# Kernel optimization log

Hardware: AMD Instinct MI355X
Metric: run time of the kernel (lower is better)

Reference implementation:

```python
import jax, jax.numpy as jnp
import numpy as np

T, OBS, MLP, H, ACT = 2048, 512, 1024, 1024, 16
SIG0 = 0.5  # config['noise_std'] -> NoisyLinear init_std


def mish(x):
    return x * jnp.tanh(jax.nn.softplus(x))


def noisy_linear(x, wm, ws, bm, bs, kw, kb):
    # NoisyLinear: perturbed weights/bias sampled per forward call from the key.
    # In the original, the same key is tiled across the vmapped time axis, so a
    # single noise sample is shared by all timesteps -> one sample here.
    w = wm + ws * jax.random.normal(kw, wm.shape, wm.dtype)
    b = bm + bs * jax.random.normal(kb, bm.shape, bm.dtype)
    return x @ w.T + b


def setup_inputs() -> dict:
    key = jax.random.key(0)
    ks = jax.random.split(key, 8)

    def lin(k, o, i):
        lim = 1.0 / np.sqrt(i)
        return jax.random.uniform(k, (o, i), jnp.float32, -lim, lim)

    return {
        "x": jax.random.normal(ks[0], (T, OBS), jnp.float32),
        "state": jnp.zeros((H,), jnp.float32),
        "start": jax.random.randint(ks[1], (T,), 0, 2, dtype=jnp.int32),
        "done": jnp.zeros((T,), jnp.int32),
        "pre_wm": lin(ks[2], MLP, OBS),
        "pre_ws": jnp.full((MLP, OBS), SIG0, jnp.float32),
        "pre_bm": jnp.zeros((MLP,), jnp.float32),
        "pre_bs": jnp.full((MLP,), SIG0, jnp.float32),
        "gru_wih": lin(ks[3], 3 * H, MLP),
        "gru_whh": lin(ks[4], 3 * H, H),
        "gru_b": jnp.zeros((3 * H,), jnp.float32),
        "gru_bn": jnp.zeros((H,), jnp.float32),
        "p1_wm": lin(ks[5], MLP, H),
        "p1_ws": jnp.full((MLP, H), SIG0, jnp.float32),
        "p1_bm": jnp.zeros((MLP,), jnp.float32),
        "p1_bs": jnp.full((MLP,), SIG0, jnp.float32),
        "p2_wm": lin(ks[6], MLP, MLP),
        "p2_ws": jnp.full((MLP, MLP), SIG0, jnp.float32),
        "p2_bm": jnp.zeros((MLP,), jnp.float32),
        "p2_bs": jnp.full((MLP,), SIG0, jnp.float32),
        "p3_wm": lin(ks[7], ACT, MLP) * 0.01,  # final_layer_init: small last layer
        "p3_ws": jnp.full((ACT, MLP), SIG0, jnp.float32),
        "p3_bm": jnp.zeros((ACT,), jnp.float32),
        "p3_bs": jnp.full((ACT,), SIG0, jnp.float32),
    }


def _forward(x, state, start, pre_wm, pre_ws, pre_bm, pre_bs, gru_wih, gru_whh,
             gru_b, gru_bn, p1_wm, p1_ws, p1_bm, p1_bs, p2_wm, p2_ws, p2_bm,
             p2_bs, p3_wm, p3_ws, p3_bm, p3_bs):
    nk = jax.random.split(jax.random.key(7), 8)
    # pre MLP: NoisyLinear + mish, vectorized over time
    z = mish(noisy_linear(x, pre_wm, pre_ws, pre_bm, pre_bs, nk[0], nk[1]))  # [T, MLP]
    # input-side GRU gates precomputed as one big GEMM (equinox GRUCell math)
    igates = z @ gru_wih.T + gru_b  # [T, 3H]
    keep = (1 - start).astype(z.dtype)  # [T]; 0 where an episode starts -> reset h

    def step(h, inp):
        ig, k = inp
        h_in = h * k  # state * logical_not(start)
        hg = h_in @ gru_whh.T  # [3H]
        ir, iz, in_ = jnp.split(ig, 3)
        hr, hz, hn = jnp.split(hg, 3)
        r = jax.nn.sigmoid(ir + hr)
        u = jax.nn.sigmoid(iz + hz)
        n = jnp.tanh(in_ + r * (hn + gru_bn))
        h_new = n + u * (h_in - n)  # == (1-u)*n + u*h_in
        return h_new, h_new

    final_state, states = jax.lax.scan(step, state, (igates, keep))  # states: [T, H]
    # post MLP: NoisyLinear+mish, NoisyLinear+mish, NoisyLinear (final)
    y = mish(noisy_linear(states, p1_wm, p1_ws, p1_bm, p1_bs, nk[2], nk[3]))
    y = mish(noisy_linear(y, p2_wm, p2_ws, p2_bm, p2_bs, nk[4], nk[5]))
    y = noisy_linear(y, p3_wm, p3_ws, p3_bm, p3_bs, nk[6], nk[7])  # [T, ACT]
    return y, final_state


def reference(x, state, start, done, pre_wm, pre_ws, pre_bm, pre_bs, gru_wih,
              gru_whh, gru_b, gru_bn, p1_wm, p1_ws, p1_bm, p1_bs, p2_wm, p2_ws,
              p2_bm, p2_bs, p3_wm, p3_ws, p3_bm, p3_bs):
    del done  # threaded through the scan in the original but never used
    return _forward(x, state, start, pre_wm, pre_ws, pre_bm, pre_bs, gru_wih,
                    gru_whh, gru_b, gru_bn, p1_wm, p1_ws, p1_bm, p1_bs, p2_wm,
                    p2_ws, p2_bm, p2_bs, p3_wm, p3_ws, p3_bm, p3_bs)
```

## Files before the change

### kernel.cpp

```cpp
#include <hip/hip_runtime.h>
#include <hip/hip_cooperative_groups.h>
#include <cstdint>
#include <cstddef>

namespace cg = cooperative_groups;

#define T_ 2048
#define OBS_ 512
#define MLP_ 1024
#define H_ 1024
#define ACT_ 16
#define H3_ 3072

typedef short bf16x8 __attribute__((ext_vector_type(8)));
typedef float f32x4 __attribute__((ext_vector_type(4)));

__host__ __device__ __forceinline__ uint32_t rotl32(uint32_t v, int d) {
  return (v << d) | (v >> (32 - d));
}
__host__ __device__ __forceinline__ void tf2x32(uint32_t k0, uint32_t k1,
                                                uint32_t x0, uint32_t x1,
                                                uint32_t& o0, uint32_t& o1) {
  uint32_t ks2 = k0 ^ k1 ^ 0x1BD11BDAu;
  x0 += k0; x1 += k1;
  x0 += x1; x1 = rotl32(x1, 13); x1 ^= x0;
  x0 += x1; x1 = rotl32(x1, 15); x1 ^= x0;
  x0 += x1; x1 = rotl32(x1, 26); x1 ^= x0;
  x0 += x1; x1 = rotl32(x1, 6);  x1 ^= x0;
  x0 += k1; x1 += ks2 + 1u;
  x0 += x1; x1 = rotl32(x1, 17); x1 ^= x0;
  x0 += x1; x1 = rotl32(x1, 29); x1 ^= x0;
  x0 += x1; x1 = rotl32(x1, 16); x1 ^= x0;
  x0 += x1; x1 = rotl32(x1, 24); x1 ^= x0;
  x0 += ks2; x1 += k0 + 2u;
  x0 += x1; x1 = rotl32(x1, 13); x1 ^= x0;
  x0 += x1; x1 = rotl32(x1, 15); x1 ^= x0;
  x0 += x1; x1 = rotl32(x1, 26); x1 ^= x0;
  x0 += x1; x1 = rotl32(x1, 6);  x1 ^= x0;
  x0 += k0; x1 += k1 + 3u;
  x0 += x1; x1 = rotl32(x1, 17); x1 ^= x0;
  x0 += x1; x1 = rotl32(x1, 29); x1 ^= x0;
  x0 += x1; x1 = rotl32(x1, 16); x1 ^= x0;
  x0 += x1; x1 = rotl32(x1, 24); x1 ^= x0;
  x0 += k1; x1 += ks2 + 4u;
  x0 += x1; x1 = rotl32(x1, 13); x1 ^= x0;
  x0 += x1; x1 = rotl32(x1, 15); x1 ^= x0;
  x0 += x1; x1 = rotl32(x1, 26); x1 ^= x0;
  x0 += x1; x1 = rotl32(x1, 6);  x1 ^= x0;
  x0 += ks2; x1 += k0 + 5u;
  o0 = x0; o1 = x1;
}

__device__ __forceinline__ float erfinv_f32(float x) {
  float w = -log1pf(-x * x);
  float p;
  if (w < 5.0f) {
    w = w - 2.5f;
    p = 2.81022636e-08f;
    p = fmaf(p, w, 3.43273939e-07f);
    p = fmaf(p, w, -3.5233877e-06f);
    p = fmaf(p, w, -4.39150654e-06f);
    p = fmaf(p, w, 0.00021858087f);
    p = fmaf(p, w, -0.00125372503f);
    p = fmaf(p, w, -0.00417768164f);
    p = fmaf(p, w, 0.246640727f);
    p = fmaf(p, w, 1.50140941f);
  } else {
    w = sqrtf(w) - 3.0f;
    p = -0.000200214257f;
    p = fmaf(p, w, 0.000100950558f);
    p = fmaf(p, w, 0.00134934322f);
    p = fmaf(p, w, -0.00367342844f);
    p = fmaf(p, w, 0.00573950773f);
    p = fmaf(p, w, -0.0076224613f);
    p = fmaf(p, w, 0.00943887047f);
    p = fmaf(p, w, 1.00167406f);
    p = fmaf(p, w, 2.83297682f);
  }
  return p * x;
}

__device__ __forceinline__ float bits_to_normal(uint32_t bits) {
  const float lo = -0.99999994f;
  float f = __uint_as_float((bits >> 9) | 0x3f800000u) - 1.0f;
  float u = fmaf(f, 2.0f, lo);
  u = fmaxf(lo, u);
  return 1.41421356237f * erfinv_f32(u);
}

__device__ __forceinline__ float sigmoidf_(float x) {
  return 1.0f / (1.0f + expf(-x));
}
__device__ __forceinline__ float mishf_(float x) {
  float sp = fmaxf(x, 0.0f) + log1pf(expf(-fabsf(x)));
  return x * tanhf(sp);
}

__device__ __forceinline__ ushort f2bf(float v) {
  uint32_t u = __float_as_uint(v);
  uint32_t r = (u + 0x7FFFu + ((u >> 16) & 1u)) >> 16;
  return (ushort)r;
}
__device__ __forceinline__ float bf2f(ushort b) {
  return __uint_as_float(((uint32_t)b) << 16);
}

struct NoiseDesc {
  const float* wm; const float* ws;
  ushort* dh; ushort* dl; float* df;
  uint32_t k0, k1, base, mode;
};
struct NoiseArgs { NoiseDesc d[8]; uint32_t total; int* meta_zero; };

__global__ __launch_bounds__(256) void k_gen_noise(NoiseArgs a) {
  if (blockIdx.x < 16) a.meta_zero[blockIdx.x * 256 + threadIdx.x] = 0;
  uint32_t idx = blockIdx.x * 256u + threadIdx.x;
  for (; idx < a.total; idx += gridDim.x * 256u) {
    int ti = 0;
#pragma unroll
    for (int i = 1; i < 8; ++i) if (idx >= a.d[i].base) ti = i;
    NoiseDesc dd = a.d[ti];
    uint32_t j = idx - dd.base;
    uint32_t b1, b2;
    tf2x32(dd.k0, dd.k1, 0u, j, b1, b2);
    float v = fmaf(dd.ws[j], bits_to_normal(b1 ^ b2), dd.wm[j]);
    if (dd.mode) {
      ushort hb = f2bf(v);
      dd.dh[j] = hb;
      dd.dl[j] = f2bf(v - bf2f(hb));
    } else {
      dd.df[j] = v;
    }
  }
}

__global__ __launch_bounds__(256) void k_split(const float* __restrict__ in,
                                               ushort* __restrict__ h,
                                               ushort* __restrict__ l, int n4) {
  int i = blockIdx.x * 256 + threadIdx.x;
  if (i >= n4) return;
  float4 v = ((const float4*)in)[i];
  ushort4 hb, lb;
  hb.x = f2bf(v.x); lb.x = f2bf(v.x - bf2f(hb.x));
  hb.y = f2bf(v.y); lb.y = f2bf(v.y - bf2f(hb.y));
  hb.z = f2bf(v.z); lb.z = f2bf(v.z - bf2f(hb.z));
  hb.w = f2bf(v.w); lb.w = f2bf(v.w - bf2f(hb.w));
  ((ushort4*)h)[i] = hb;
  ((ushort4*)l)[i] = lb;
}

template <int ACTF, int OUTM>
__global__ __launch_bounds__(256, 2) void k_mgemm(
    const ushort* __restrict__ Ah, const ushort* __restrict__ Al,
    const ushort* __restrict__ Wh, const ushort* __restrict__ Wl,
    const float* __restrict__ bias,
    float* __restrict__ Cf, ushort* __restrict__ Ch, ushort* __restrict__ Cl,
    int K, int Nreal, int ldc) {
  __shared__ ushort sA[2][128 * 32];
  __shared__ ushort sW[2][128 * 32];
  const int tid = threadIdx.x;
  const int m0 = blockIdx.y * 128, n0 = blockIdx.x * 128;
  const int wid = tid >> 6, lane = tid & 63;
  const int wm = (wid >> 1) * 64, wn = (wid & 1) * 64;
  const int lr = lane & 15, lk = lane >> 4;
  const int r0 = tid >> 2;
  const int c0 = (tid & 3) * 8;
  f32x4 acc[4][4] = {};
  for (int k0 = 0; k0 < K; k0 += 32) {
    const size_t aoff0 = (size_t)(m0 + r0) * K + k0 + c0;
    const size_t aoff1 = (size_t)(m0 + r0 + 64) * K + k0 + c0;
    const size_t woff0 = (size_t)(n0 + r0) * K + k0 + c0;
    const size_t woff1 = (size_t)(n0 + r0 + 64) * K + k0 + c0;
    int4 ah0 = *(const int4*)(Ah + aoff0);
    int4 ah1 = *(const int4*)(Ah + aoff1);
    int4 al0 = *(const int4*)(Al + aoff0);
    int4 al1 = *(const int4*)(Al + aoff1);
    int4 wh0 = *(const int4*)(Wh + woff0);
    int4 wh1 = *(const int4*)(Wh + woff1);
    int4 wl0 = *(const int4*)(Wl + woff0);
    int4 wl1 = *(const int4*)(Wl + woff1);
    __syncthreads();
    *(int4*)(&sA[0][r0 * 32 + c0]) = ah0;
    *(int4*)(&sA[0][(r0 + 64) * 32 + c0]) = ah1;
    *(int4*)(&sA[1][r0 * 32 + c0]) = al0;
    *(int4*)(&sA[1][(r0 + 64) * 32 + c0]) = al1;
    *(int4*)(&sW[0][r0 * 32 + c0]) = wh0;
    *(int4*)(&sW[0][(r0 + 64) * 32 + c0]) = wh1;
    *(int4*)(&sW[1][r0 * 32 + c0]) = wl0;
    *(int4*)(&sW[1][(r0 + 64) * 32 + c0]) = wl1;
    __syncthreads();
    bf16x8 fah[4], fal[4], fwh[4], fwl[4];
#pragma unroll
    for (int f = 0; f < 4; ++f) {
      int ar = (wm + f * 16 + lr) * 32 + lk * 8;
      fah[f] = *(const bf16x8*)(&sA[0][ar]);
      fal[f] = *(const bf16x8*)(&sA[1][ar]);
      int wr = (wn + f * 16 + lr) * 32 + lk * 8;
      fwh[f] = *(const bf16x8*)(&sW[0][wr]);
      fwl[f] = *(const bf16x8*)(&sW[1][wr]);
    }
#pragma unroll
    for (int mf = 0; mf < 4; ++mf)
#pragma unroll
      for (int nf = 0; nf < 4; ++nf) {
        acc[mf][nf] = __builtin_amdgcn_mfma_f32_16x16x32_bf16(fah[mf], fwh[nf], acc[mf][nf], 0, 0, 0);
        acc[mf][nf] = __builtin_amdgcn_mfma_f32_16x16x32_bf16(fah[mf], fwl[nf], acc[mf][nf], 0, 0, 0);
        acc[mf][nf] = __builtin_amdgcn_mfma_f32_16x16x32_bf16(fal[mf], fwh[nf], acc[mf][nf], 0, 0, 0);
      }
  }
#pragma unroll
  for (int mf = 0; mf < 4; ++mf)
#pragma unroll
    for (int nf = 0; nf < 4; ++nf) {
      int col = n0 + wn + nf * 16 + lr;
      if (col >= Nreal) continue;
      float bv = bias[col];
#pragma unroll
      for (int r = 0; r < 4; ++r) {
        int row = m0 + wm + mf * 16 + lk * 4 + r;
        float v = acc[mf][nf][r] + bv;
        if (ACTF) v = mishf_(v);
        if (OUTM == 0) {
          Cf[(size_t)row * ldc + col] = v;
        } else {
          ushort hb = f2bf(v);
          Ch[(size_t)row * ldc + col] = hb;
          Cl[(size_t)row * ldc + col] = f2bf(v - bf2f(hb));
        }
      }
    }
}

struct SMemScan {
  union {
    struct {
      ushort Hs[2][64][40];
      ushort Bs[2][96][40];
    } mm;
    int scan[2][2048];
  } u;
  int tl[64];
};

__global__ __launch_bounds__(256) void k_scan(
    const float* __restrict__ ig, const float* __restrict__ whh,
    const float* __restrict__ gbn, const float* __restrict__ state0,
    const int* __restrict__ start, int* __restrict__ counts,
    int* __restrict__ cursors, int* __restrict__ li_,
    int* __restrict__ offsets, int* __restrict__ list,
    ushort* __restrict__ st_h, ushort* __restrict__ st_l,
    float* __restrict__ hg0) {
  cg::grid_group grid = cg::this_grid();
  __shared__ SMemScan sm;
  const int tid = threadIdx.x, bid = blockIdx.x, nb = gridDim.x;
  const float keep0 = 1.0f - (float)start[0];

  if (bid < 8) {
    int t = bid * 256 + tid;
    int l = 0, tt = t;
    while (tt > 0 && start[tt] == 0) { tt--; l++; }
    li_[t] = l;
    if (t > 0) atomicAdd(&counts[l], 1);
  }
  grid.sync();

  if (bid == 0) {
    for (int i = tid; i < 2048; i += 256) sm.u.scan[0][i] = counts[i];
    __syncthreads();
    int cur = 0;
    for (int d = 1; d < 2048; d <<= 1) {
      int nx = cur ^ 1;
      for (int i = tid; i < 2048; i += 256)
        sm.u.scan[nx][i] = sm.u.scan[cur][i] + (i >= d ? sm.u.scan[cur][i - d] : 0);
      __syncthreads();
      cur = nx;
    }
    for (int i = tid; i < 2048; i += 256)
      offsets[i] = (i == 0) ? 0 : sm.u.scan[cur][i - 1];
  }
  grid.sync();

  if (bid < 8) {
    int t = bid * 256 + tid;
    if (t > 0) {
      int l = li_[t];
      int pos = atomicAdd(&cursors[l], 1);
      list[offsets[l] + pos] = t;
    }
  }
  {
    int gw = bid * 4 + (tid >> 6);
    int lane = tid & 63;
    for (int r = gw * 3; r < gw * 3 + 3 && r < H3_; ++r) {
      const float* wr = whh + (size_t)r * H_;
      float s = 0.f;
      for (int c = lane; c < H_; c += 64) s = fmaf(wr[c], state0[c] * keep0, s);
      for (int o = 32; o; o >>= 1) s += __shfl_down(s, o, 64);
      if (lane == 0) hg0[r] = s;
    }
  }
  grid.sync();

  {
    int cnt0 = counts[0];
    int off0 = offsets[0];
    int total = (cnt0 + 1) * H_;
    for (int e = bid * 256 + tid; e < total; e += nb * 256) {
      int s = e >> 10, i = e & (H_ - 1);
      int t; float hin, hr, hz, hn;
      if (s == 0) {
        t = 0; hin = state0[i] * keep0;
        hr = hg0[i]; hz = hg0[H_ + i]; hn = hg0[2 * H_ + i];
      } else {
        t = list[off0 + s - 1]; hin = 0.f; hr = 0.f; hz = 0.f; hn = 0.f;
      }
      float ir = ig[(size_t)t * H3_ + i];
      float iz = ig[(size_t)t * H3_ + H_ + i];
      float in_ = ig[(size_t)t * H3_ + 2 * H_ + i];
      float r = sigmoidf_(ir + hr), u = sigmoidf_(iz + hz);
      float n = tanhf(in_ + r * (hn + gbn[i]));
      float v = n + u * (hin - n);
      ushort hb = f2bf(v);
      st_h[(size_t)t * H_ + i] = hb;
      st_l[(size_t)t * H_ + i] = f2bf(v - bf2f(hb));
    }
  }
  grid.sync();

  const int wid = tid >> 6, lane = tid & 63;
  const int lr = lane & 15, lk = lane >> 4;
  const int wm = (wid >> 1) * 32;
  const int wi = wid & 1;

  for (int k = 1; k < 2048; ++k) {
    int cnt = counts[k];
    if (cnt == 0) break;
    int off = offsets[k];
    int mtiles = (cnt + 63) >> 6;
    int tiles = mtiles << 5;
    for (int tile = bid; tile < tiles; tile += nb) {
      int mt = tile >> 5;
      int i0 = (tile & 31) << 5;
      __syncthreads();
      if (tid < 64) {
        int s = mt * 64 + tid;
        sm.tl[tid] = (s < cnt) ? list[off + s] : 0;
      }
      __syncthreads();

      f32x4 acc[2][3] = {};
      int4 pa[2]; float4 pb[3];
      const int a_koct = tid & 3, a_row = (tid >> 2) & 63;
      const int b_kq0 = tid & 7, b_row0 = tid >> 3;
      const int b_kq1 = (tid + 256) & 7, b_row1 = (tid + 256) >> 3;
      const int b_kq2 = (tid + 512) & 7, b_row2 = (tid + 512) >> 3;
      const size_t brow_off0 = (size_t)(((b_row0 >> 5) * H_) + i0 + (b_row0 & 31)) * H_;
      const size_t brow_off1 = (size_t)(((b_row1 >> 5) * H_) + i0 + (b_row1 & 31)) * H_;
      const size_t brow_off2 = (size_t)(((b_row2 >> 5) * H_) + i0 + (b_row2 & 31)) * H_;

#define LOADA(K0, DST)                                                        \
      {                                                                       \
        int t0_ = sm.tl[a_row];                                               \
        DST[0] = make_int4(0, 0, 0, 0); DST[1] = make_int4(0, 0, 0, 0);       \
        if (t0_ > 0) {                                                        \
          size_t base_ = (size_t)(t0_ - 1) * H_ + (K0) + a_koct * 8;          \
          DST[0] = *(const int4*)(st_h + base_);                              \
          DST[1] = *(const int4*)(st_l + base_);                              \
        }                                                                     \
      }
#define LOADB(K0, DST)                                                        \
      {                                                                       \
        DST[0] = *(const float4*)(whh + brow_off0 + (K0) + b_kq0 * 4);        \
        DST[1] = *(const float4*)(whh + brow_off1 + (K0) + b_kq1 * 4);        \
        DST[2] = *(const float4*)(whh + brow_off2 + (K0) + b_kq2 * 4);        \
      }

      LOADA(0, pa); LOADB(0, pb);
      for (int k0 = 0; k0 < H_; k0 += 32) {
        __syncthreads();
        *(int4*)(&sm.u.mm.Hs[0][a_row][a_koct * 8]) = pa[0];
        *(int4*)(&sm.u.mm.Hs[1][a_row][a_koct * 8]) = pa[1];
        {
          ushort4 hb, lb;
          float4 w = pb[0];
          hb.x = f2bf(w.x); lb.x = f2bf(w.x - bf2f(hb.x));
          hb.y = f2bf(w.y); lb.y = f2bf(w.y - bf2f(hb.y));
          hb.z = f2bf(w.z); lb.z = f2bf(w.z - bf2f(hb.z));
          hb.w = f2bf(w.w); lb.w = f2bf(w.w - bf2f(hb.w));
          *(ushort4*)(&sm.u.mm.Bs[0][b_row0][b_kq0 * 4]) = hb;
          *(ushort4*)(&sm.u.mm.Bs[1][b_row0][b_kq0 * 4]) = lb;
          w = pb[1];
          hb.x = f2bf(w.x); lb.x = f2bf(w.x - bf2f(hb.x));
          hb.y = f2bf(w.y); lb.y = f2bf(w.y - bf2f(hb.y));
          hb.z = f2bf(w.z); lb.z = f2bf(w.z - bf2f(hb.z));
          hb.w = f2bf(w.w); lb.w = f2bf(w.w - bf2f(hb.w));
          *(ushort4*)(&sm.u.mm.Bs[0][b_row1][b_kq1 * 4]) = hb;
          *(ushort4*)(&sm.u.mm.Bs[1][b_row1][b_kq1 * 4]) = lb;
          w = pb[2];
          hb.x = f2bf(w.x); lb.x = f2bf(w.x - bf2f(hb.x));
          hb.y = f2bf(w.y); lb.y = f2bf(w.y - bf2f(hb.y));
          hb.z = f2bf(w.z); lb.z = f2bf(w.z - bf2f(hb.z));
          hb.w = f2bf(w.w); lb.w = f2bf(w.w - bf2f(hb.w));
          *(ushort4*)(&sm.u.mm.Bs[0][b_row2][b_kq2 * 4]) = hb;
          *(ushort4*)(&sm.u.mm.Bs[1][b_row2][b_kq2 * 4]) = lb;
        }
        int4 na[2] = {pa[0], pa[1]};
        float4 nb[3] = {pb[0], pb[1], pb[2]};
        if (k0 + 32 < H_) { LOADA(k0 + 32, na); LOADB(k0 + 32, nb); }
        __syncthreads();
        bf16x8 ah[2], al[2], bh[3], bl[3];
#pragma unroll
        for (int mf = 0; mf < 2; ++mf) {
          int row = wm + mf * 16 + lr;
          ah[mf] = *(const bf16x8*)(&sm.u.mm.Hs[0][row][lk * 8]);
          al[mf] = *(const bf16x8*)(&sm.u.mm.Hs[1][row][lk * 8]);
        }
#pragma unroll
        for (int g = 0; g < 3; ++g) {
          int row = g * 32 + wi * 16 + lr;
          bh[g] = *(const bf16x8*)(&sm.u.mm.Bs[0][row][lk * 8]);
          bl[g] = *(const bf16x8*)(&sm.u.mm.Bs[1][row][lk * 8]);
        }
#pragma unroll
        for (int mf = 0; mf < 2; ++mf)
#pragma unroll
          for (int g = 0; g < 3; ++g) {
            acc[mf][g] = __builtin_amdgcn_mfma_f32_16x16x32_bf16(ah[mf], bh[g], acc[mf][g], 0, 0, 0);
            acc[mf][g] = __builtin_amdgcn_mfma_f32_16x16x32_bf16(ah[mf], bl[g], acc[mf][g], 0, 0, 0);
            acc[mf][g] = __builtin_amdgcn_mfma_f32_16x16x32_bf16(al[mf], bh[g], acc[mf][g], 0, 0, 0);
          }
        pa[0] = na[0]; pa[1] = na[1];
        pb[0] = nb[0]; pb[1] = nb[1]; pb[2] = nb[2];
      }
#undef LOADA
#undef LOADB
      int i = i0 + wi * 16 + lr;
#pragma unroll
      for (int mf = 0; mf < 2; ++mf)
#pragma unroll
        for (int r = 0; r < 4; ++r) {
          int slot = wm + mf * 16 + lk * 4 + r;
          int t = sm.tl[slot];
          if (t <= 0) continue;
          size_t pidx = (size_t)(t - 1) * H_ + i;
          float hin = bf2f(st_h[pidx]) + bf2f(st_l[pidx]);
          float ir = ig[(size_t)t * H3_ + i];
          float iz = ig[(size_t)t * H3_ + H_ + i];
          float in_ = ig[(size_t)t * H3_ + 2 * H_ + i];
          float rr = sigmoidf_(ir + acc[mf][0][r]);
          float uu = sigmoidf_(iz + acc[mf][1][r]);
          float nn = tanhf(in_ + rr * (acc[mf][2][r] + gbn[i]));
          float v = nn + uu * (hin - nn);
          ushort hb = f2bf(v);
          st_h[(size_t)t * H_ + i] = hb;
          st_l[(size_t)t * H_ + i] = f2bf(v - bf2f(hb));
        }
    }
    grid.sync();
  }
}

__global__ void k_final(const ushort* __restrict__ st_h,
                        const ushort* __restrict__ st_l,
                        float* __restrict__ out) {
  int i = blockIdx.x * 256 + threadIdx.x;
  if (i < H_)
    out[T_ * ACT_ + i] = bf2f(st_h[(size_t)(T_ - 1) * H_ + i]) +
                         bf2f(st_l[(size_t)(T_ - 1) * H_ + i]);
}

extern "C" void kernel_launch(void* const* d_in, const int* in_sizes, int n_in,
                              void* d_out, int out_size, void* d_ws, size_t ws_size,
                              hipStream_t stream) {
  const float* x      = (const float*)d_in[0];
  const float* state0 = (const float*)d_in[1];
  const int*   start  = (const int*)d_in[2];
  const float* pre_wm = (const float*)d_in[4];
  const float* pre_ws = (const float*)d_in[5];
  const float* pre_bm = (const float*)d_in[6];
  const float* pre_bs = (const float*)d_in[7];
  const float* gru_wih = (const float*)d_in[8];
  const float* gru_whh = (const float*)d_in[9];
  const float* gru_b  = (const float*)d_in[10];
  const float* gru_bn = (const float*)d_in[11];
  const float* p1_wm = (const float*)d_in[12];
  const float* p1_ws = (const float*)d_in[13];
  const float* p1_bm = (const float*)d_in[14];
  const float* p1_bs = (const float*)d_in[15];
  const float* p2_wm = (const float*)d_in[16];
  const float* p2_ws = (const float*)d_in[17];
  const float* p2_bm = (const float*)d_in[18];
  const float* p2_bs = (const float*)d_in[19];
  const float* p3_wm = (const float*)d_in[20];
  const float* p3_ws = (const float*)d_in[21];
  const float* p3_bm = (const float*)d_in[22];
  const float* p3_bs = (const float*)d_in[23];

  char* p = (char*)d_ws;
  auto nxt = [&](size_t bytes) { char* r = p; p += (bytes + 255) & ~255ul; return r; };
  ushort* wihh = (ushort*)nxt((size_t)H3_ * MLP_ * 2);
  ushort* wihl = (ushort*)nxt((size_t)H3_ * MLP_ * 2);
  ushort* preWh = (ushort*)nxt((size_t)MLP_ * OBS_ * 2);
  ushort* preWl = (ushort*)nxt((size_t)MLP_ * OBS_ * 2);
  ushort* p1Wh = (ushort*)nxt((size_t)MLP_ * H_ * 2);
  ushort* p1Wl = (ushort*)nxt((size_t)MLP_ * H_ * 2);
  ushort* p2Wh = (ushort*)nxt((size_t)MLP_ * MLP_ * 2);
  ushort* p2Wl = (ushort*)nxt((size_t)MLP_ * MLP_ * 2);
  ushort* p3Wh = (ushort*)nxt((size_t)128 * MLP_ * 2);
  ushort* p3Wl = (ushort*)nxt((size_t)128 * MLP_ * 2);
  float* preB = (float*)nxt(MLP_ * 4);
  float* p1B  = (float*)nxt(MLP_ * 4);
  float* p2B  = (float*)nxt(MLP_ * 4);
  float* p3B  = (float*)nxt(ACT_ * 4);
  ushort* B1h = (ushort*)nxt((size_t)T_ * MLP_ * 2);
  ushort* B1l = (ushort*)nxt((size_t)T_ * MLP_ * 2);
  ushort* B2h = (ushort*)nxt((size_t)T_ * MLP_ * 2);
  ushort* B2l = (ushort*)nxt((size_t)T_ * MLP_ * 2);
  float* igb = (float*)nxt((size_t)T_ * H3_ * 4);
  float* hg0 = (float*)nxt(H3_ * 4);
  int* counts  = (int*)nxt(2048 * 4);
  int* cursors = (int*)nxt(2048 * 4);
  int* li      = (int*)nxt(2048 * 4);
  int* offsets = (int*)nxt(2048 * 4);
  int* list    = (int*)nxt(2048 * 4);

  uint32_t nk0[8], nk1[8];
  for (int i = 0; i < 8; ++i) {
    uint32_t b1, b2;
    tf2x32(0u, 7u, 0u, (uint32_t)i, b1, b2);
    nk0[i] = b1; nk1[i] = b2;
  }

  NoiseArgs na;
  const float* wms[8] = {pre_wm, pre_bm, p1_wm, p1_bm, p2_wm, p2_bm, p3_wm, p3_bm};
  const float* wss[8] = {pre_ws, pre_bs, p1_ws, p1_bs, p2_ws, p2_bs, p3_ws, p3_bs};
  ushort* dhs[8] = {preWh, nullptr, p1Wh, nullptr, p2Wh, nullptr, p3Wh, nullptr};
  ushort* dls[8] = {preWl, nullptr, p1Wl, nullptr, p2Wl, nullptr, p3Wl, nullptr};
  float* dfs[8]  = {nullptr, preB, nullptr, p1B, nullptr, p2B, nullptr, p3B};
  uint32_t ns[8] = {MLP_ * OBS_, MLP_, MLP_ * H_, MLP_, MLP_ * MLP_, MLP_, ACT_ * MLP_, ACT_};
  uint32_t base = 0;
  for (int i = 0; i < 8; ++i) {
    na.d[i].wm = wms[i]; na.d[i].ws = wss[i];
    na.d[i].dh = dhs[i]; na.d[i].dl = dls[i]; na.d[i].df = dfs[i];
    na.d[i].k0 = nk0[i]; na.d[i].k1 = nk1[i];
    na.d[i].base = base; na.d[i].mode = (i & 1) ? 0u : 1u;
    base += ns[i];
  }
  na.total = base;
  na.meta_zero = counts;

  dim3 b256(256);

  hipMemsetAsync(p3Wh + 16 * MLP_, 0, (size_t)112 * MLP_ * 2, stream);
  hipMemsetAsync(p3Wl + 16 * MLP_, 0, (size_t)112 * MLP_ * 2, stream);

  k_gen_noise<<<dim3(4096), b256, 0, stream>>>(na);
  k_split<<<dim3((H3_ * MLP_ / 4) / 256), b256, 0, stream>>>(gru_wih, wihh, wihl, H3_ * MLP_ / 4);
  k_split<<<dim3((T_ * OBS_ / 4) / 256), b256, 0, stream>>>(x, B2h, B2l, T_ * OBS_ / 4);

  k_mgemm<1, 1><<<dim3(MLP_ / 128, T_ / 128), b256, 0, stream>>>(
      B2h, B2l, preWh, preWl, preB, nullptr, B1h, B1l, OBS_, MLP_, MLP_);
  k_mgemm<0, 0><<<dim3(H3_ / 128, T_ / 128), b256, 0, stream>>>(
      B1h, B1l, wihh, wihl, gru_b, igb, nullptr, nullptr, MLP_, H3_, H3_);

  {
    const float* a0 = igb; const float* a1 = gru_whh; const float* a2 = gru_bn;
    const float* a3 = state0; const int* a4 = start;
    int* a5 = counts; int* a6 = cursors; int* a7 = li; int* a8 = offsets; int* a9 = list;
    ushort* a10 = B2h; ushort* a11 = B2l; float* a12 = hg0;
    void* args[] = {&a0, &a1, &a2, &a3, &a4, &a5, &a6, &a7, &a8, &a9, &a10, &a11, &a12};
    hipLaunchCooperativeKernel((void*)k_scan, dim3(256), dim3(256), args, 0, stream);
  }

  k_final<<<dim3(4), b256, 0, stream>>>(B2h, B2l, (float*)d_out);

  k_mgemm<1, 1><<<dim3(MLP_ / 128, T_ / 128), b256, 0, stream>>>(
      B2h, B2l, p1Wh, p1Wl, p1B, nullptr, B1h, B1l, H_, MLP_, MLP_);
  k_mgemm<1, 1><<<dim3(MLP_ / 128, T_ / 128), b256, 0, stream>>>(
      B1h, B1l, p2Wh, p2Wl, p2B, nullptr, B2h, B2l, MLP_, MLP_, MLP_);
  k_mgemm<0, 0><<<dim3(1, T_ / 128), b256, 0, stream>>>(
      B2h, B2l, p3Wh, p3Wl, p3B, (float*)d_out, nullptr, nullptr, MLP_, ACT_, ACT_);
}
```

Measured before the change: 1.207 ms.

## Pre-split recurrent weights to bf16 pairs, double-buffer scan GEMM, widen scan grid

Adds a k_split pass that turns gru_whh into bf16 high/low arrays (reusing the wihh/wihl buffers) before the cooperative scan. Inside the scan, B tiles are now loaded directly as int4 bf16 data instead of being converted from fp32 on every tile. The K loop is unrolled by two with ping-pong register prefetch. The cooperative grid is also sized from the occupancy query, up to 4 blocks per CU instead of a fixed 256 blocks. The goal is to remove the per-step conversion ALU work and raise parallelism in the latency-bound sequential scan. In exchange it adds an extra split kernel and more grid.sync participants.

```diff
diff --git a/kernel.cpp b/kernel.cpp
--- a/kernel.cpp
+++ b/kernel.cpp
@@ -243,7 +243,8 @@
 };
 
 __global__ __launch_bounds__(256) void k_scan(
-    const float* __restrict__ ig, const float* __restrict__ whh,
+    const float* __restrict__ ig, const float* __restrict__ whhf,
+    const ushort* __restrict__ whh_h, const ushort* __restrict__ whh_l,
     const float* __restrict__ gbn, const float* __restrict__ state0,
     const int* __restrict__ start, int* __restrict__ counts,
     int* __restrict__ cursors, int* __restrict__ li_,
@@ -292,7 +293,7 @@
     int gw = bid * 4 + (tid >> 6);
     int lane = tid & 63;
     for (int r = gw * 3; r < gw * 3 + 3 && r < H3_; ++r) {
-      const float* wr = whh + (size_t)r * H_;
+      const float* wr = whhf + (size_t)r * H_;
       float s = 0.f;
       for (int c = lane; c < H_; c += 64) s = fmaf(wr[c], state0[c] * keep0, s);
       for (int o = 32; o; o >>= 1) s += __shfl_down(s, o, 64);
@@ -331,6 +332,20 @@
   const int lr = lane & 15, lk = lane >> 4;
   const int wm = (wid >> 1) * 32;
   const int wi = wid & 1;
+
+  const int a_koct = tid & 3, a_row = (tid >> 2) & 63;
+  int blev[3], brow[3], bkoct[3];
+#pragma unroll
+  for (int j = 0; j < 3; ++j) {
+    int c = tid + 256 * j;
+    blev[j] = c / 384;
+    int rem = c - blev[j] * 384;
+    brow[j] = rem >> 2;
+    bkoct[j] = rem & 3;
+  }
+  const ushort* bsp[3];
+#pragma unroll
+  for (int j = 0; j < 3; ++j) bsp[j] = blev[j] ? whh_l : whh_h;
 
   for (int k = 1; k < 2048; ++k) {
     int cnt = counts[k];
@@ -348,15 +363,13 @@
       }
       __syncthreads();
 
+      size_t bsrc[3];
+#pragma unroll
+      for (int j = 0; j < 3; ++j)
+        bsrc[j] = (size_t)((brow[j] >> 5) * H_ + i0 + (brow[j] & 31)) * H_ + bkoct[j] * 8;
+
       f32x4 acc[2][3] = {};
-      int4 pa[2]; float4 pb[3];
-      const int a_koct = tid & 3, a_row = (tid >> 2) & 63;
-      const int b_kq0 = tid & 7, b_row0 = tid >> 3;
-      const int b_kq1 = (tid + 256) & 7, b_row1 = (tid + 256) >> 3;
-      const int b_kq2 = (tid + 512) & 7, b_row2 = (tid + 512) >> 3;
-      const size_t brow_off0 = (size_t)(((b_row0 >> 5) * H_) + i0 + (b_row0 & 31)) * H_;
-      const size_t brow_off1 = (size_t)(((b_row1 >> 5) * H_) + i0 + (b_row1 & 31)) * H_;
-      const size_t brow_off2 = (size_t)(((b_row2 >> 5) * H_) + i0 + (b_row2 & 31)) * H_;
+      int4 paA[2], paB[2], pbA[3], pbB[3];
 
 #define LOADA(K0, DST)                                                        \
       {                                                                       \
@@ -370,70 +383,61 @@
       }
 #define LOADB(K0, DST)                                                        \
       {                                                                       \
-        DST[0] = *(const float4*)(whh + brow_off0 + (K0) + b_kq0 * 4);        \
-        DST[1] = *(const float4*)(whh + brow_off1 + (K0) + b_kq1 * 4);        \
-        DST[2] = *(const float4*)(whh + brow_off2 + (K0) + b_kq2 * 4);        \
-      }
-
-      LOADA(0, pa); LOADB(0, pb);
-      for (int k0 = 0; k0 < H_; k0 += 32) {
+        _Pragma("unroll")                                                     \
+        for (int j = 0; j < 3; ++j)                                           \
+          DST[j] = *(const int4*)(bsp[j] + bsrc[j] + (K0));                   \
+      }
+#define WRITEAB(PA, PB)                                                       \
+      {                                                                       \
+        *(int4*)(&sm.u.mm.Hs[0][a_row][a_koct * 8]) = PA[0];                  \
+        *(int4*)(&sm.u.mm.Hs[1][a_row][a_koct * 8]) = PA[1];                  \
+        _Pragma("unroll")                                                     \
+        for (int j = 0; j < 3; ++j)                                           \
+          *(int4*)(&sm.u.mm.Bs[blev[j]][brow[j]][bkoct[j] * 8]) = PB[j];      \
+      }
+#define COMPUTE()                                                             \
+      {                                                                       \
+        bf16x8 ah[2], al[2], bh[3], bl[3];                                    \
+        _Pragma("unroll")                                                     \
+        for (int mf = 0; mf < 2; ++mf) {                                      \
+          int row = wm + mf * 16 + lr;                                        \
+          ah[mf] = *(const bf16x8*)(&sm.u.mm.Hs[0][row][lk * 8]);             \
+          al[mf] = *(const bf16x8*)(&sm.u.mm.Hs[1][row][lk * 8]);             \
+        }                                                                     \
+        _Pragma("unroll")                                                     \
+        for (int g = 0; g < 3; ++g) {                                         \
+          int row = g * 32 + wi * 16 + lr;                                    \
+          bh[g] = *(const bf16x8*)(&sm.u.mm.Bs[0][row][lk * 8]);              \
+          bl[g] = *(const bf16x8*)(&sm.u.mm.Bs[1][row][lk * 8]);              \
+        }                                                                     \
+        _Pragma("unroll")                                                     \
+        for (int mf = 0; mf < 2; ++mf)                                        \
+          _Pragma("unroll")                                                   \
+          for (int g = 0; g < 3; ++g) {                                       \
+            acc[mf][g] = __builtin_amdgcn_mfma_f32_16x16x32_bf16(ah[mf], bh[g], acc[mf][g], 0, 0, 0); \
+            acc[mf][g] = __builtin_amdgcn_mfma_f32_16x16x32_bf16(ah[mf], bl[g], acc[mf][g], 0, 0, 0); \
+            acc[mf][g] = __builtin_amdgcn_mfma_f32_16x16x32_bf16(al[mf], bh[g], acc[mf][g], 0, 0, 0); \
+          }                                                                   \
+      }
+
+      LOADA(0, paA); LOADB(0, pbA);
+      LOADA(32, paB); LOADB(32, pbB);
+      for (int k0 = 0; k0 < H_; k0 += 64) {
         __syncthreads();
-        *(int4*)(&sm.u.mm.Hs[0][a_row][a_koct * 8]) = pa[0];
-        *(int4*)(&sm.u.mm.Hs[1][a_row][a_koct * 8]) = pa[1];
-        {
-          ushort4 hb, lb;
-          float4 w = pb[0];
-          hb.x = f2bf(w.x); lb.x = f2bf(w.x - bf2f(hb.x));
-          hb.y = f2bf(w.y); lb.y = f2bf(w.y - bf2f(hb.y));
-          hb.z = f2bf(w.z); lb.z = f2bf(w.z - bf2f(hb.z));
-          hb.w = f2bf(w.w); lb.w = f2bf(w.w - bf2f(hb.w));
-          *(ushort4*)(&sm.u.mm.Bs[0][b_row0][b_kq0 * 4]) = hb;
-          *(ushort4*)(&sm.u.mm.Bs[1][b_row0][b_kq0 * 4]) = lb;
-          w = pb[1];
-          hb.x = f2bf(w.x); lb.x = f2bf(w.x - bf2f(hb.x));
-          hb.y = f2bf(w.y); lb.y = f2bf(w.y - bf2f(hb.y));
-          hb.z = f2bf(w.z); lb.z = f2bf(w.z - bf2f(hb.z));
-          hb.w = f2bf(w.w); lb.w = f2bf(w.w - bf2f(hb.w));
-          *(ushort4*)(&sm.u.mm.Bs[0][b_row1][b_kq1 * 4]) = hb;
-          *(ushort4*)(&sm.u.mm.Bs[1][b_row1][b_kq1 * 4]) = lb;
-          w = pb[2];
-          hb.x = f2bf(w.x); lb.x = f2bf(w.x - bf2f(hb.x));
-          hb.y = f2bf(w.y); lb.y = f2bf(w.y - bf2f(hb.y));
-          hb.z = f2bf(w.z); lb.z = f2bf(w.z - bf2f(hb.z));
-          hb.w = f2bf(w.w); lb.w = f2bf(w.w - bf2f(hb.w));
-          *(ushort4*)(&sm.u.mm.Bs[0][b_row2][b_kq2 * 4]) = hb;
-          *(ushort4*)(&sm.u.mm.Bs[1][b_row2][b_kq2 * 4]) = lb;
-        }
-        int4 na[2] = {pa[0], pa[1]};
-        float4 nb[3] = {pb[0], pb[1], pb[2]};
-        if (k0 + 32 < H_) { LOADA(k0 + 32, na); LOADB(k0 + 32, nb); }
+        WRITEAB(paA, pbA);
+        if (k0 + 64 < H_) { LOADA(k0 + 64, paA); LOADB(k0 + 64, pbA); }
         __syncthreads();
-        bf16x8 ah[2], al[2], bh[3], bl[3];
-#pragma unroll
-        for (int mf = 0; mf < 2; ++mf) {
-          int row = wm + mf * 16 + lr;
-          ah[mf] = *(const bf16x8*)(&sm.u.mm.Hs[0][row][lk * 8]);
-          al[mf] = *(const bf16x8*)(&sm.u.mm.Hs[1][row][lk * 8]);
-        }
-#pragma unroll
-        for (int g = 0; g < 3; ++g) {
-          int row = g * 32 + wi * 16 + lr;
-          bh[g] = *(const bf16x8*)(&sm.u.mm.Bs[0][row][lk * 8]);
-          bl[g] = *(const bf16x8*)(&sm.u.mm.Bs[1][row][lk * 8]);
-        }
-#pragma unroll
-        for (int mf = 0; mf < 2; ++mf)
-#pragma unroll
-          for (int g = 0; g < 3; ++g) {
-            acc[mf][g] = __builtin_amdgcn_mfma_f32_16x16x32_bf16(ah[mf], bh[g], acc[mf][g], 0, 0, 0);
-            acc[mf][g] = __builtin_amdgcn_mfma_f32_16x16x32_bf16(ah[mf], bl[g], acc[mf][g], 0, 0, 0);
-            acc[mf][g] = __builtin_amdgcn_mfma_f32_16x16x32_bf16(al[mf], bh[g], acc[mf][g], 0, 0, 0);
-          }
-        pa[0] = na[0]; pa[1] = na[1];
-        pb[0] = nb[0]; pb[1] = nb[1]; pb[2] = nb[2];
+        COMPUTE();
+        __syncthreads();
+        WRITEAB(paB, pbB);
+        if (k0 + 96 < H_) { LOADA(k0 + 96, paB); LOADB(k0 + 96, pbB); }
+        __syncthreads();
+        COMPUTE();
       }
 #undef LOADA
 #undef LOADB
+#undef WRITEAB
+#undef COMPUTE
       int i = i0 + wi * 16 + lr;
 #pragma unroll
       for (int mf = 0; mf < 2; ++mf)
@@ -563,13 +567,22 @@
   k_mgemm<0, 0><<<dim3(H3_ / 128, T_ / 128), b256, 0, stream>>>(
       B1h, B1l, wihh, wihl, gru_b, igb, nullptr, nullptr, MLP_, H3_, H3_);
 
+  k_split<<<dim3((H3_ * H_ / 4) / 256), b256, 0, stream>>>(gru_whh, wihh, wihl, H3_ * H_ / 4);
+
   {
-    const float* a0 = igb; const float* a1 = gru_whh; const float* a2 = gru_bn;
-    const float* a3 = state0; const int* a4 = start;
-    int* a5 = counts; int* a6 = cursors; int* a7 = li; int* a8 = offsets; int* a9 = list;
-    ushort* a10 = B2h; ushort* a11 = B2l; float* a12 = hg0;
-    void* args[] = {&a0, &a1, &a2, &a3, &a4, &a5, &a6, &a7, &a8, &a9, &a10, &a11, &a12};
-    hipLaunchCooperativeKernel((void*)k_scan, dim3(256), dim3(256), args, 0, stream);
+    int maxb = 0;
+    if (hipOccupancyMaxActiveBlocksPerMultiprocessor(&maxb, (const void*)k_scan, 256, 0)
+            != hipSuccess || maxb < 1)
+      maxb = 1;
+    if (maxb > 4) maxb = 4;
+    const float* a0 = igb; const float* a1 = gru_whh;
+    const ushort* a2 = wihh; const ushort* a3 = wihl;
+    const float* a4 = gru_bn; const float* a5 = state0; const int* a6 = start;
+    int* a7 = counts; int* a8 = cursors; int* a9 = li; int* a10 = offsets; int* a11 = list;
+    ushort* a12 = B2h; ushort* a13 = B2l; float* a14 = hg0;
+    void* args[] = {&a0, &a1, &a2, &a3, &a4, &a5, &a6, &a7, &a8, &a9,
+                    &a10, &a11, &a12, &a13, &a14};
+    hipLaunchCooperativeKernel((void*)k_scan, dim3(256 * maxb), dim3(256), args, 0, stream);
   }
 
   k_final<<<dim3(4), b256, 0, stream>>>(B2h, B2l, (float*)d_out);
```

Result: slower. 1.608 ms (+33.3%).
